# Performance work log

Hardware: AMD Instinct MI355X
Metric: run time of the kernel (lower is better)

The kernel has to match this reference:

```python
import jax, jax.numpy as jnp
import numpy as np

THRESHOLD = 0.5     # overlap_thresh
NEG_POS = 3         # negative:positive ratio
VAR = (0.1, 0.2)    # cfg['variance']


def point_form(pr):
    # cxcywh -> xmin,ymin,xmax,ymax
    return jnp.concatenate([pr[:, :2] - pr[:, 2:] / 2, pr[:, :2] + pr[:, 2:] / 2], axis=1)


def jaccard(a, b):
    # a: [N,4] point-form truths, b: [P,4] point-form priors -> IoU [N,P]
    lt = jnp.maximum(a[:, None, :2], b[None, :, :2])
    rb = jnp.minimum(a[:, None, 2:], b[None, :, 2:])
    wh = jnp.clip(rb - lt, 0.0)
    inter = wh[..., 0] * wh[..., 1]
    area_a = ((a[:, 2] - a[:, 0]) * (a[:, 3] - a[:, 1]))[:, None]
    area_b = ((b[:, 2] - b[:, 0]) * (b[:, 3] - b[:, 1]))[None, :]
    return inter / (area_a + area_b - inter)


def encode(matched, priors):
    # matched: [P,4] point-form, priors: [P,4] cxcywh
    g_cxcy = ((matched[:, :2] + matched[:, 2:]) / 2 - priors[:, :2]) / (VAR[0] * priors[:, 2:])
    g_wh = jnp.log((matched[:, 2:] - matched[:, :2]) / priors[:, 2:]) / VAR[1]
    return jnp.concatenate([g_cxcy, g_wh], axis=1)


def match_one(truths, labels, priors):
    # truths [N,4], labels [N], priors [P,4] cxcywh
    N = truths.shape[0]
    P = priors.shape[0]
    overlaps = jaccard(truths, point_form(priors))          # [N,P]
    best_prior_idx = jnp.argmax(overlaps, axis=1)           # [N] best prior per truth
    best_truth_overlap = jnp.max(overlaps, axis=0)          # [P]
    best_truth_idx = jnp.argmax(overlaps, axis=0)           # [P]
    # ensure each truth's best prior is kept (overlap forced to 2)
    best_truth_overlap = best_truth_overlap.at[best_prior_idx].set(2.0)
    hit = best_prior_idx[:, None] == jnp.arange(P)[None, :]  # [N,P]
    chosen = jnp.max(jnp.where(hit, jnp.arange(N)[:, None], -1), axis=0)
    best_truth_idx = jnp.where(chosen >= 0, chosen, best_truth_idx)
    matched = truths[best_truth_idx]                        # [P,4]
    conf = labels[best_truth_idx].astype(jnp.int32) + 1
    conf = jnp.where(best_truth_overlap < THRESHOLD, 0, conf)
    return encode(matched, priors), conf


def smooth_l1(x):
    ax = jnp.abs(x)
    return jnp.where(ax < 1.0, 0.5 * ax * ax, ax - 0.5)


def multibox_loss(loc_data, conf_data, priors, targets):
    num, P, C = conf_data.shape
    truths = targets[..., :4]
    labels = targets[..., 4]
    loc_t, conf_t = jax.vmap(match_one, in_axes=(0, 0, None))(truths, labels, priors)
    pos = conf_t > 0                                        # [B,P]

    # localization loss over positives
    loss_l = jnp.sum(jnp.where(pos[..., None], smooth_l1(loc_data - loc_t), 0.0))

    # hard-negative mining score: logsumexp - conf[label clamped to {0,1}]
    batch_conf = jax.lax.stop_gradient(conf_data).reshape(-1, C)
    conf_flat = conf_t.reshape(-1)
    clamped = jnp.where(conf_flat != 0, 1, conf_flat)
    # replicate torch nonzero()-indexing quirk: row 0 also set to 1 if any positive exists
    clamped = clamped.at[0].set(jnp.where(jnp.any(conf_flat != 0), 1, clamped[0]))
    lse = jax.scipy.special.logsumexp(batch_conf, axis=1)
    loss_c = lse - jnp.take_along_axis(batch_conf, clamped[:, None], axis=1)[:, 0]
    loss_c = loss_c.reshape(num, P)
    loss_c = jnp.where(pos, 0.0, loss_c)
    # rank of each prior by descending mining loss
    idx_rank = jnp.argsort(jnp.argsort(-loss_c, axis=1), axis=1)
    num_pos = jnp.sum(pos.astype(jnp.int32), axis=1, keepdims=True)  # [B,1]
    num_neg = jnp.clip(NEG_POS * num_pos, None, P - 1)
    neg = idx_rank < num_neg
    sel = pos | neg

    # confidence cross-entropy over selected priors, original labels as targets
    logp = jax.nn.log_softmax(conf_data, axis=-1)           # [B,P,C]
    ce = -jnp.take_along_axis(logp, conf_t[..., None], axis=-1)[..., 0]
    loss_conf = jnp.sum(jnp.where(sel, ce, 0.0))

    Nf = jnp.sum(num_pos).astype(jnp.float32)
    return loss_l / Nf, loss_conf / Nf


def setup_inputs() -> dict:
    key = jax.random.key(0)
    k1, k2, k3, k4, k5, k6, k7 = jax.random.split(key, 7)
    B, P, C, NOBJ = 128, 8732, 21, 20
    loc_data = jax.random.normal(k1, (B, P, 4), jnp.float32)
    conf_data = jax.random.normal(k2, (B, P, C), jnp.float32)
    pcxy = jax.random.uniform(k3, (P, 2), jnp.float32, 0.05, 0.95)
    pwh = jax.random.uniform(k4, (P, 2), jnp.float32, 0.05, 0.4)
    priors = jnp.concatenate([pcxy, pwh], axis=1)           # cxcywh
    mins = jax.random.uniform(k5, (B, NOBJ, 2), jnp.float32, 0.0, 0.6)
    wh = jax.random.uniform(k6, (B, NOBJ, 2), jnp.float32, 0.05, 0.35)
    lab = jax.random.randint(k7, (B, NOBJ), 0, C - 1).astype(jnp.float32)
    targets = jnp.concatenate([mins, mins + wh, lab[..., None]], axis=-1)
    return {"loc_data": loc_data, "conf_data": conf_data, "priors": priors, "targets": targets}


def reference(loc_data, conf_data, priors, targets):
    return multibox_loss(loc_data, conf_data, priors, targets)
```

## Files before the change

kernel.cpp:

```cpp
#include <hip/hip_runtime.h>

#define PP 8732
#define NB 20
#define NC 21
#define BTH 256
#define CHP 512
#define NCH 18
#define BTS 1024
#define NWS (BTS/64)

__device__ __forceinline__ float sl1(float d){
  float a = fabsf(d);
  return a < 1.0f ? 0.5f*a*a : a - 0.5f;
}

__device__ __forceinline__ float wave_max64(float x){
  int t;
  t = __builtin_amdgcn_update_dpp(0, __float_as_int(x), 0x111, 0xF, 0xF, true); x = fmaxf(x, __int_as_float(t));
  t = __builtin_amdgcn_update_dpp(0, __float_as_int(x), 0x112, 0xF, 0xF, true); x = fmaxf(x, __int_as_float(t));
  t = __builtin_amdgcn_update_dpp(0, __float_as_int(x), 0x114, 0xF, 0xF, true); x = fmaxf(x, __int_as_float(t));
  t = __builtin_amdgcn_update_dpp(0, __float_as_int(x), 0x118, 0xF, 0xF, true); x = fmaxf(x, __int_as_float(t));
  t = __builtin_amdgcn_update_dpp(0, __float_as_int(x), 0x142, 0xF, 0xF, true); x = fmaxf(x, __int_as_float(t));
  t = __builtin_amdgcn_update_dpp(0, __float_as_int(x), 0x143, 0xF, 0xF, true); x = fmaxf(x, __int_as_float(t));
  return __int_as_float(__builtin_amdgcn_readlane(__float_as_int(x), 63));
}

__device__ __forceinline__ int wave_sum64_lane63(int x){
  x += __builtin_amdgcn_update_dpp(0, x, 0x111, 0xF, 0xF, true);
  x += __builtin_amdgcn_update_dpp(0, x, 0x112, 0xF, 0xF, true);
  x += __builtin_amdgcn_update_dpp(0, x, 0x114, 0xF, 0xF, true);
  x += __builtin_amdgcn_update_dpp(0, x, 0x118, 0xF, 0xF, true);
  x += __builtin_amdgcn_update_dpp(0, x, 0x142, 0xF, 0xF, true);
  x += __builtin_amdgcn_update_dpp(0, x, 0x143, 0xF, 0xF, true);
  return x;
}

extern "C" __global__ void __launch_bounds__(BTH, 6)
mb_main(const float* __restrict__ conf_data,
        const float* __restrict__ priors,
        const float* __restrict__ targets,
        float* __restrict__ rankneg,
        unsigned char* __restrict__ meta,
        unsigned long long* __restrict__ keys2)
{
  const int b = blockIdx.x, chunk = blockIdx.y;
  const int tid = threadIdx.x, lane = tid & 63, wid = tid >> 6;
  const int q0w = chunk*CHP + wid*128;
  const int p0  = q0w + 2*lane;

  __shared__ unsigned long long s_keys[4][NB];

  float tx=0.f, ty=0.f, tz=0.f, tw=0.f;
  if (lane < NB){
    const float* tp = targets + ((long)b*NB + lane)*5;
    tx = tp[0]; ty = tp[1]; tz = tp[2]; tw = tp[3];
  }
  const float area_a = (tz-tx)*(tw-ty);

  unsigned long long mykey = 0ULL;

  if (q0w < PP){
    float bx1[2], by1[2], bx2[2], by2[2], areab[2];
    #pragma unroll
    for (int i=0;i<2;i++){
      int p = p0 + i;
      int pc = (p < PP) ? p : 0;
      float4 pr = reinterpret_cast<const float4*>(priors)[pc];
      float x1 = pr.x - pr.z*0.5f, y1 = pr.y - pr.w*0.5f;
      float x2 = pr.x + pr.z*0.5f, y2 = pr.y + pr.w*0.5f;
      if (p >= PP){ x1=3e9f; y1=3e9f; x2=3e9f; y2=3e9f; }
      bx1[i]=x1; by1[i]=y1; bx2[i]=x2; by2[i]=y2;
      areab[i] = (x2-x1)*(y2-y1);
    }

    float bestov[2] = {-1.f,-1.f};
    int   bestn [2] = {0,0};

    #pragma unroll
    for (int n=0;n<NB;n++){
      float t_x = __int_as_float(__builtin_amdgcn_readlane(__float_as_int(tx), n));
      float t_y = __int_as_float(__builtin_amdgcn_readlane(__float_as_int(ty), n));
      float t_z = __int_as_float(__builtin_amdgcn_readlane(__float_as_int(tz), n));
      float t_w = __int_as_float(__builtin_amdgcn_readlane(__float_as_int(tw), n));
      float aa  = __int_as_float(__builtin_amdgcn_readlane(__float_as_int(area_a), n));
      float candiou = -1.0f; unsigned candp = 0u;
      #pragma unroll
      for (int i=0;i<2;i++){
        float lx=fmaxf(t_x,bx1[i]), ly=fmaxf(t_y,by1[i]);
        float rx=fminf(t_z,bx2[i]), ry=fminf(t_w,by2[i]);
        float iw=fmaxf(rx-lx,0.f), ih=fmaxf(ry-ly,0.f);
        float inter = iw*ih;
        float iou = inter * __builtin_amdgcn_rcpf(aa + areab[i] - inter);
        if (iou > bestov[i]){ bestov[i]=iou; bestn[i]=n; }
        if (iou > candiou){ candiou=iou; candp=(unsigned)(p0+i); }
      }
      float wmax = wave_max64(candiou);
      unsigned long long mk = __ballot(candiou == wmax);
      int wlane = __ffsll((long long)mk) - 1;
      unsigned wp = (unsigned)__builtin_amdgcn_readlane((int)candp, wlane);
      unsigned long long key = ((unsigned long long)__float_as_uint(wmax)<<32)
                             | (unsigned long long)(0xFFFFFFFFu - wp);
      if (lane == n) mykey = key;
    }

    if (p0 < PP){
      float rr2[2];
      unsigned metab = 0u;
      #pragma unroll
      for (int i=0;i<2;i++){
        const float* cb = conf_data + ((long)b*PP + p0 + i)*NC;
        const float4* cb4 = reinterpret_cast<const float4*>(cb);
        float4 ca0=cb4[0], ca1=cb4[1], ca2=cb4[2], ca3=cb4[3], ca4=cb4[4];
        float c20 = cb[20];
        float vv[NC] = {ca0.x,ca0.y,ca0.z,ca0.w, ca1.x,ca1.y,ca1.z,ca1.w,
                        ca2.x,ca2.y,ca2.z,ca2.w, ca3.x,ca3.y,ca3.z,ca3.w,
                        ca4.x,ca4.y,ca4.z,ca4.w, c20};
        float m = vv[0];
        #pragma unroll
        for (int c=1;c<NC;c++) m = fmaxf(m, vv[c]);
        float s = 0.f;
        #pragma unroll
        for (int c=0;c<NC;c++) s += __expf(vv[c]-m);
        float lse = __logf(s) + m;
        rr2[i] = lse - vv[0];
        metab |= ((unsigned)((bestn[i]<<1) | (bestov[i] >= 0.5f ? 1 : 0))) << (8*i);
      }
      *reinterpret_cast<float2*>(rankneg + (long)b*PP + p0) = make_float2(rr2[0], rr2[1]);
      *reinterpret_cast<unsigned short*>(meta + (long)b*PP + p0) =
          (unsigned short)(metab & 0xFFFFu);
    }
  }

  if (lane < NB) s_keys[wid][lane] = mykey;
  __syncthreads();
  if (tid < NB){
    unsigned long long mx = s_keys[0][tid];
    #pragma unroll
    for (int w=1;w<4;w++) if (s_keys[w][tid] > mx) mx = s_keys[w][tid];
    keys2[((long)b*NCH + chunk)*NB + tid] = mx;
  }
}

extern "C" __global__ void __launch_bounds__(BTS)
mb_select(const float* __restrict__ loc_data,
          const float* __restrict__ conf_data,
          const float* __restrict__ priors,
          const float* __restrict__ targets,
          const float* __restrict__ rankneg,
          const unsigned char* __restrict__ meta,
          const unsigned long long* __restrict__ keys2,
          float* __restrict__ rowres, int* __restrict__ ticket,
          float* __restrict__ out, int Bn)
{
  const int b = blockIdx.x, tid = threadIdx.x, lane = tid & 63, wid = tid >> 6;
  __shared__ __align__(16) float s_val[PP];
  __shared__ __align__(16) unsigned int s_meta4[PP/4];
  __shared__ float4 s_tr4[NB];
  __shared__ float s_lab[NB];
  __shared__ int   s_bp[NB];
  __shared__ int   s_tot[32];
  __shared__ float s_fa[NWS], s_fb[NWS], s_fc[NWS];
  __shared__ int   s_ia[NWS];
  __shared__ float s_rowll, s_rowpc;
  __shared__ int   s_npos, s_last;
  unsigned char* s_meta = (unsigned char*)s_meta4;
  float4* sv4 = reinterpret_cast<float4*>(s_val);

  const float4* rr = reinterpret_cast<const float4*>(rankneg + (long)b*PP);
  for (int i=tid;i<PP/4;i+=BTS) sv4[i]=rr[i];
  const unsigned int* mr = reinterpret_cast<const unsigned int*>(meta + (long)b*PP);
  for (int i=tid;i<PP/4;i+=BTS) s_meta4[i]=mr[i];
  if (tid < NB*5){
    int n = tid/5, k2 = tid-n*5;
    float vv = targets[((long)b*NB+n)*5+k2];
    if (k2<4) ((float*)&s_tr4[n])[k2]=vv; else s_lab[n]=vv;
  }
  if (tid < NB){
    unsigned long long mx = 0ULL;
    #pragma unroll
    for (int c=0;c<NCH;c++){
      unsigned long long kk = keys2[((long)b*NCH + c)*NB + tid];
      if (kk > mx) mx = kk;
    }
    s_bp[tid] = (int)(0xFFFFFFFFu - (unsigned)(mx & 0xFFFFFFFFULL));
  }
  if (tid < 32) s_tot[tid] = 0;
  __syncthreads();

  if (tid==0){
    for (int n=0;n<NB;n++) s_meta[s_bp[n]] = (unsigned char)((n<<1)|1);
  }
  __syncthreads();

  float4 rv0 = sv4[tid];
  float4 rv1 = sv4[tid+1024];
  float4 rv2 = (tid < PP/4-2048) ? sv4[tid+2048] : make_float4(0.f,0.f,0.f,0.f);
  unsigned mm0 = s_meta4[tid];
  unsigned mm1 = s_meta4[tid+1024];
  unsigned mm2 = (tid < PP/4-2048) ? s_meta4[tid+2048] : 0u;
  if (mm0 & 0x00000001u) rv0.x = 0.f;
  if (mm0 & 0x00000100u) rv0.y = 0.f;
  if (mm0 & 0x00010000u) rv0.z = 0.f;
  if (mm0 & 0x01000000u) rv0.w = 0.f;
  if (mm1 & 0x00000001u) rv1.x = 0.f;
  if (mm1 & 0x00000100u) rv1.y = 0.f;
  if (mm1 & 0x00010000u) rv1.z = 0.f;
  if (mm1 & 0x01000000u) rv1.w = 0.f;
  if (mm2 & 0x00000001u) rv2.x = 0.f;
  if (mm2 & 0x00000100u) rv2.y = 0.f;
  if (mm2 & 0x00010000u) rv2.z = 0.f;
  if (mm2 & 0x01000000u) rv2.w = 0.f;

  int spec = 0; float delta = 0.f, val0 = 0.f;
  if (b==0 && tid==0 && !(mm0 & 1u)){
    float v0 = conf_data[0], v1 = conf_data[1];
    float r0 = rv0.x;
    float r0p = r0 + v0 - v1;
    delta = r0 - r0p;
    spec = 1;
    rv0.x = r0p; val0 = r0p;
  }

  float ll=0.f, pc=0.f; int np=0;
  for (int p=tid;p<PP;p+=BTS){
    int mt = s_meta[p];
    if (mt & 1){
      np++;
      int n = mt>>1;
      int ct = (int)s_lab[n] + 1;
      const float* cp = conf_data + ((long)b*PP+p)*NC;
      float v0 = cp[0], vct = cp[ct];
      pc += s_val[p] + v0 - vct;
      float4 t = s_tr4[n];
      float4 prr = reinterpret_cast<const float4*>(priors)[p];
      float4 ld = reinterpret_cast<const float4*>(loc_data)[(long)b*PP+p];
      float g0 = ((t.x+t.z)*0.5f - prr.x)/(0.1f*prr.z);
      float g1 = ((t.y+t.w)*0.5f - prr.y)/(0.1f*prr.w);
      float g2 = __logf((t.z-t.x)/prr.z)/0.2f;
      float g3 = __logf((t.w-t.y)/prr.w)/0.2f;
      ll += sl1(ld.x-g0)+sl1(ld.y-g1)+sl1(ld.z-g2)+sl1(ld.w-g3);
    }
  }
  #pragma unroll
  for (int o=32;o;o>>=1){
    ll += __shfl_down(ll,o,64);
    pc += __shfl_down(pc,o,64);
    np += __shfl_down(np,o,64);
  }
  if (lane==0){ s_fa[wid]=ll; s_fb[wid]=pc; s_ia[wid]=np; }
  __syncthreads();
  if (tid==0){
    float a=0.f,c2=0.f; int ni=0;
    for (int w=0;w<NWS;w++){ a+=s_fa[w]; c2+=s_fb[w]; ni+=s_ia[w]; }
    s_rowll=a; s_rowpc=c2; s_npos=ni;
  }
  __syncthreads();
  const int num_pos = s_npos;
  int k = num_pos*3; if (k > PP-1) k = PP-1;

  float negsum = 0.f;
  if (k > 0){
    unsigned lo=0u, hi=0x7f800000u;
    int it=0;
    while (lo < hi){
      unsigned mid = lo + ((hi - lo + 1u) >> 1);
      int c = (__float_as_uint(rv0.x)>=mid) + (__float_as_uint(rv0.y)>=mid)
            + (__float_as_uint(rv0.z)>=mid) + (__float_as_uint(rv0.w)>=mid)
            + (__float_as_uint(rv1.x)>=mid) + (__float_as_uint(rv1.y)>=mid)
            + (__float_as_uint(rv1.z)>=mid) + (__float_as_uint(rv1.w)>=mid)
            + (__float_as_uint(rv2.x)>=mid) + (__float_as_uint(rv2.y)>=mid)
            + (__float_as_uint(rv2.z)>=mid) + (__float_as_uint(rv2.w)>=mid);
      c = wave_sum64_lane63(c);
      if (lane==63) atomicAdd(&s_tot[it], c);
      __syncthreads();
      int tot = s_tot[it];
      if (tot >= k) lo = mid; else hi = mid - 1u;
      it++;
    }
    const unsigned vstar = lo;

    int cg=0; float sg=0.f;
    #define ACC(x) if (__float_as_uint(x)>vstar){cg++;sg+=(x);}
    ACC(rv0.x) ACC(rv0.y) ACC(rv0.z) ACC(rv0.w)
    ACC(rv1.x) ACC(rv1.y) ACC(rv1.z) ACC(rv1.w)
    ACC(rv2.x) ACC(rv2.y) ACC(rv2.z) ACC(rv2.w)
    #undef ACC
    #pragma unroll
    for (int o=32;o;o>>=1){ cg += __shfl_down(cg,o,64); sg += __shfl_down(sg,o,64); }
    __syncthreads();
    if (lane==0){ s_ia[wid]=cg; s_fa[wid]=sg; }
    __syncthreads();
    if (tid==0){
      int cG=0; float sumG=0.f;
      for (int w=0;w<NWS;w++){ cG+=s_ia[w]; sumG+=s_fa[w]; }
      int tie = k - cG;
      negsum = sumG + (float)tie * __uint_as_float(vstar);
      if (b==0 && spec && __float_as_uint(val0) >= vstar) negsum += delta;
    }
  }

  if (tid==0){
    rowres[b*4+0] = s_rowll;
    rowres[b*4+1] = s_rowpc + negsum;
    rowres[b*4+2] = (float)num_pos;
    __threadfence();
    int t = atomicAdd(ticket, 1);
    s_last = (t == Bn - 1) ? 1 : 0;
  }
  __syncthreads();

  if (s_last){
    __threadfence();
    float a0=0.f, a1=0.f, a2=0.f;
    for (int i=tid;i<Bn;i+=BTS){
      a0 += rowres[i*4+0]; a1 += rowres[i*4+1]; a2 += rowres[i*4+2];
    }
    #pragma unroll
    for (int o=32;o;o>>=1){
      a0 += __shfl_down(a0,o,64);
      a1 += __shfl_down(a1,o,64);
      a2 += __shfl_down(a2,o,64);
    }
    if (lane==0){ s_fa[wid]=a0; s_fb[wid]=a1; s_fc[wid]=a2; }
    __syncthreads();
    if (tid==0){
      float A0=0.f,A1=0.f,A2=0.f;
      for (int w=0;w<NWS;w++){ A0+=s_fa[w]; A1+=s_fb[w]; A2+=s_fc[w]; }
      out[0] = A0/A2;
      out[1] = A1/A2;
    }
  }
}

extern "C" void kernel_launch(void* const* d_in, const int* in_sizes, int n_in,
                              void* d_out, int out_size, void* d_ws, size_t ws_size,
                              hipStream_t stream) {
  const float* loc     = (const float*)d_in[0];
  const float* conf    = (const float*)d_in[1];
  const float* priors  = (const float*)d_in[2];
  const float* targets = (const float*)d_in[3];
  float* out = (float*)d_out;
  int B = in_sizes[0] / (PP*4);

  char* ws = (char*)d_ws;
  int*   ticket = (int*)ws;
  float* rowres = (float*)(ws + 64);
  unsigned long long* keys2 = (unsigned long long*)(ws + 4096);
  size_t off_rank = (4096 + (size_t)B*NCH*NB*8 + 255) & ~(size_t)255;
  float* rankneg = (float*)(ws + off_rank);
  unsigned char* metaa = (unsigned char*)(ws + off_rank + (size_t)B*PP*4);

  hipMemsetAsync(d_ws, 0, 64, stream);
  hipLaunchKernelGGL(mb_main,   dim3(B, NCH), dim3(BTH), 0, stream,
                     conf, priors, targets, rankneg, metaa, keys2);
  hipLaunchKernelGGL(mb_select, dim3(B), dim3(BTS), 0, stream,
                     loc, conf, priors, targets, rankneg, metaa, keys2,
                     rowres, ticket, out, B);
}
```

Baseline: 199.4 us.

## Split fused match/LSE kernel into separate LSE and matching kernels

The fused main kernel is split into two launches. One computes the per-prior log-sum-exp rank loss with one thread per prior. The other does only the IoU matching, reading truth boxes as uniform scalar loads instead of readlane broadcasts. The aim is to separate the memory-bound conf read from the ALU-bound matching and raise occupancy for each. The cost is an extra kernel launch, and the two phases can no longer overlap within one kernel.

After: 217.2 us. 1.09x slower.

```diff
diff --git a/kernel.cpp b/kernel.cpp
--- a/kernel.cpp
+++ b/kernel.cpp
@@ -6,6 +6,7 @@
 #define BTH 256
 #define CHP 512
 #define NCH 18
+#define NLS 35
 #define BTS 1024
 #define NWS (BTS/64)
 
@@ -35,13 +36,34 @@
   return x;
 }
 
-extern "C" __global__ void __launch_bounds__(BTH, 6)
-mb_main(const float* __restrict__ conf_data,
-        const float* __restrict__ priors,
-        const float* __restrict__ targets,
-        float* __restrict__ rankneg,
-        unsigned char* __restrict__ meta,
-        unsigned long long* __restrict__ keys2)
+extern "C" __global__ void __launch_bounds__(BTH, 8)
+mb_lse(const float* __restrict__ conf_data,
+       float* __restrict__ rankneg)
+{
+  const int b = blockIdx.x;
+  const int p = blockIdx.y*BTH + threadIdx.x;
+  if (p >= PP) return;
+  const float* cb = conf_data + ((long)b*PP + p)*NC;
+  const float4* cb4 = reinterpret_cast<const float4*>(cb);
+  float4 ca0=cb4[0], ca1=cb4[1], ca2=cb4[2], ca3=cb4[3], ca4=cb4[4];
+  float c20 = cb[20];
+  float vv[NC] = {ca0.x,ca0.y,ca0.z,ca0.w, ca1.x,ca1.y,ca1.z,ca1.w,
+                  ca2.x,ca2.y,ca2.z,ca2.w, ca3.x,ca3.y,ca3.z,ca3.w,
+                  ca4.x,ca4.y,ca4.z,ca4.w, c20};
+  float m = vv[0];
+  #pragma unroll
+  for (int c=1;c<NC;c++) m = fmaxf(m, vv[c]);
+  float s = 0.f;
+  #pragma unroll
+  for (int c=0;c<NC;c++) s += __expf(vv[c]-m);
+  rankneg[(long)b*PP + p] = __logf(s) + m - vv[0];
+}
+
+extern "C" __global__ void __launch_bounds__(BTH, 8)
+mb_match(const float* __restrict__ priors,
+         const float* __restrict__ targets,
+         unsigned char* __restrict__ meta,
+         unsigned long long* __restrict__ keys2)
 {
   const int b = blockIdx.x, chunk = blockIdx.y;
   const int tid = threadIdx.x, lane = tid & 63, wid = tid >> 6;
@@ -50,12 +72,7 @@
 
   __shared__ unsigned long long s_keys[4][NB];
 
-  float tx=0.f, ty=0.f, tz=0.f, tw=0.f;
-  if (lane < NB){
-    const float* tp = targets + ((long)b*NB + lane)*5;
-    tx = tp[0]; ty = tp[1]; tz = tp[2]; tw = tp[3];
-  }
-  const float area_a = (tz-tx)*(tw-ty);
+  const float* tb = targets + (long)b*NB*5;
 
   unsigned long long mykey = 0ULL;
 
@@ -78,11 +95,11 @@
 
     #pragma unroll
     for (int n=0;n<NB;n++){
-      float t_x = __int_as_float(__builtin_amdgcn_readlane(__float_as_int(tx), n));
-      float t_y = __int_as_float(__builtin_amdgcn_readlane(__float_as_int(ty), n));
-      float t_z = __int_as_float(__builtin_amdgcn_readlane(__float_as_int(tz), n));
-      float t_w = __int_as_float(__builtin_amdgcn_readlane(__float_as_int(tw), n));
-      float aa  = __int_as_float(__builtin_amdgcn_readlane(__float_as_int(area_a), n));
+      const float t_x = tb[n*5+0];
+      const float t_y = tb[n*5+1];
+      const float t_z = tb[n*5+2];
+      const float t_w = tb[n*5+3];
+      const float aa  = (t_z-t_x)*(t_w-t_y);
       float candiou = -1.0f; unsigned candp = 0u;
       #pragma unroll
       for (int i=0;i<2;i++){
@@ -104,30 +121,10 @@
     }
 
     if (p0 < PP){
-      float rr2[2];
-      unsigned metab = 0u;
-      #pragma unroll
-      for (int i=0;i<2;i++){
-        const float* cb = conf_data + ((long)b*PP + p0 + i)*NC;
-        const float4* cb4 = reinterpret_cast<const float4*>(cb);
-        float4 ca0=cb4[0], ca1=cb4[1], ca2=cb4[2], ca3=cb4[3], ca4=cb4[4];
-        float c20 = cb[20];
-        float vv[NC] = {ca0.x,ca0.y,ca0.z,ca0.w, ca1.x,ca1.y,ca1.z,ca1.w,
-                        ca2.x,ca2.y,ca2.z,ca2.w, ca3.x,ca3.y,ca3.z,ca3.w,
-                        ca4.x,ca4.y,ca4.z,ca4.w, c20};
-        float m = vv[0];
-        #pragma unroll
-        for (int c=1;c<NC;c++) m = fmaxf(m, vv[c]);
-        float s = 0.f;
-        #pragma unroll
-        for (int c=0;c<NC;c++) s += __expf(vv[c]-m);
-        float lse = __logf(s) + m;
-        rr2[i] = lse - vv[0];
-        metab |= ((unsigned)((bestn[i]<<1) | (bestov[i] >= 0.5f ? 1 : 0))) << (8*i);
-      }
-      *reinterpret_cast<float2*>(rankneg + (long)b*PP + p0) = make_float2(rr2[0], rr2[1]);
-      *reinterpret_cast<unsigned short*>(meta + (long)b*PP + p0) =
-          (unsigned short)(metab & 0xFFFFu);
+      unsigned short mb =
+          (unsigned short)( ((bestn[0]<<1) | (bestov[0] >= 0.5f ? 1 : 0))
+                          | (((bestn[1]<<1) | (bestov[1] >= 0.5f ? 1 : 0)) << 8) );
+      *reinterpret_cast<unsigned short*>(meta + (long)b*PP + p0) = mb;
     }
   }
 
@@ -351,8 +348,10 @@
   unsigned char* metaa = (unsigned char*)(ws + off_rank + (size_t)B*PP*4);
 
   hipMemsetAsync(d_ws, 0, 64, stream);
-  hipLaunchKernelGGL(mb_main,   dim3(B, NCH), dim3(BTH), 0, stream,
-                     conf, priors, targets, rankneg, metaa, keys2);
+  hipLaunchKernelGGL(mb_lse,    dim3(B, NLS), dim3(BTH), 0, stream,
+                     conf, rankneg);
+  hipLaunchKernelGGL(mb_match,  dim3(B, NCH), dim3(BTH), 0, stream,
+                     priors, targets, metaa, keys2);
   hipLaunchKernelGGL(mb_select, dim3(B), dim3(BTS), 0, stream,
                      loc, conf, priors, targets, rankneg, metaa, keys2,
                      rowres, ticket, out, B);
```
